# Kernel tuning notes

Measured on AMD Instinct MI355X. Metric: run time of the kernel, lower is better.

Reference implementation:

```python
import jax, jax.numpy as jnp
import numpy as np

HEADS = 8
KEY_DIM = 32
EPS = 1e-5


def layernorm(x, gamma, beta, eps=EPS):
    mu = jnp.mean(x, axis=-1, keepdims=True)
    var = jnp.mean(jnp.square(x - mu), axis=-1, keepdims=True)
    return (x - mu) * jax.lax.rsqrt(var + eps) * gamma + beta


def setup_inputs() -> dict:
    key = jax.random.key(0)
    ks = jax.random.split(key, 6)
    B, H, W, C = 16, 32, 32, 256
    inner = HEADS * KEY_DIM  # 256
    s = 1.0 / np.sqrt(C)
    return {
        "x": jax.random.normal(ks[0], (B, H, W, C), jnp.float32),
        "gamma": jnp.ones((C,), jnp.float32),
        "beta": jnp.zeros((C,), jnp.float32),
        "Wq": jax.random.normal(ks[1], (C, inner), jnp.float32) * s,
        "bq": jnp.zeros((inner,), jnp.float32),
        "Wk": jax.random.normal(ks[2], (C, inner), jnp.float32) * s,
        "bk": jnp.zeros((inner,), jnp.float32),
        "Wv": jax.random.normal(ks[3], (C, inner), jnp.float32) * s,
        "bv": jnp.zeros((inner,), jnp.float32),
        "Wp": jax.random.normal(ks[4], (inner, C), jnp.float32) * s,
        "bp": jnp.zeros((C,), jnp.float32),
    }


def reference(x, gamma, beta, Wq, bq, Wk, bk, Wv, bv, Wp, bp):
    B, H, W, C = x.shape
    N = H * W
    h, d = HEADS, KEY_DIM
    X = layernorm(x, gamma, beta)              # [B,H,W,C]
    Xf = X.reshape(B, N, C)                    # 1x1 conv == per-token linear
    Q = (Xf @ Wq + bq).reshape(B, N, h, d)
    K = (Xf @ Wk + bk).reshape(B, N, h, d)
    V = (Xf @ Wv + bv).reshape(B, N, h, d)
    scale = jnp.asarray(d, x.dtype) ** -0.5
    scores = jnp.einsum('bnhd,bmhd->bhnm', Q, K) * scale
    A = jax.nn.softmax(scores, axis=-1)        # [B,h,N,N]
    Y = jnp.einsum('bhnm,bmhd->bnhd', A, V).reshape(B, N, h * d)
    out = (Y @ Wp + bp).reshape(B, H, W, C)
    return out
```

## Files before the change

kernel.cpp:

```cpp
#include <hip/hip_runtime.h>
#include <hip/hip_bf16.h>

typedef __bf16 bf16_t;
typedef __attribute__((ext_vector_type(8))) __bf16 bf16x8;
typedef __attribute__((ext_vector_type(4))) float f32x4;
typedef __attribute__((ext_vector_type(4))) short s16x4;

#define GLDS16(g, l) __builtin_amdgcn_global_load_lds( \
    (const __attribute__((address_space(1))) unsigned int*)(g), \
    (__attribute__((address_space(3))) unsigned int*)(l), 16, 0, 0)

__device__ __forceinline__ float fexp2(float x) {
#if __has_builtin(__builtin_amdgcn_exp2f)
  return __builtin_amdgcn_exp2f(x);
#else
  return exp2f(x);
#endif
}

#define QSCALE (0.17677669529663688f * 1.4426950408889634f)

__global__ __launch_bounds__(256) void lnwtr_kernel(
    const float* __restrict__ x, const float* __restrict__ gamma,
    const float* __restrict__ beta, bf16_t* __restrict__ Xln,
    const float* __restrict__ Wq, const float* __restrict__ Wk,
    const float* __restrict__ Wv, const float* __restrict__ Wp,
    bf16_t* __restrict__ Wt)
{
  if (blockIdx.x < 1024) {
    const int idx = blockIdx.x * 256 + threadIdx.x;
    const int mat = idx >> 16;
    const int e   = idx & 65535;
    const int k   = e >> 8;
    const int n   = e & 255;
    const float* W = (mat == 0) ? Wq : (mat == 1) ? Wk : (mat == 2) ? Wv : Wp;
    Wt[(size_t)mat * 65536 + n * 256 + k] = (bf16_t)W[e];
    return;
  }
  const int wave = threadIdx.x >> 6, lane = threadIdx.x & 63;
  const int tok = (blockIdx.x - 1024) * 4 + wave;
  const float4 v = *reinterpret_cast<const float4*>(x + (size_t)tok * 256 + lane * 4);
  float s1 = v.x + v.y + v.z + v.w;
  float s2 = v.x*v.x + v.y*v.y + v.z*v.z + v.w*v.w;
  #pragma unroll
  for (int off = 1; off < 64; off <<= 1) {
    s1 += __shfl_xor(s1, off);
    s2 += __shfl_xor(s2, off);
  }
  const float mean = s1 * (1.0f/256.0f);
  const float var  = s2 * (1.0f/256.0f) - mean*mean;
  const float rstd = rsqrtf(var + 1e-5f);
  const float4 g  = *reinterpret_cast<const float4*>(gamma + lane*4);
  const float4 be = *reinterpret_cast<const float4*>(beta  + lane*4);
  union { bf16_t h4[4]; unsigned long long u; } pk;
  pk.h4[0] = (bf16_t)((v.x-mean)*rstd*g.x + be.x);
  pk.h4[1] = (bf16_t)((v.y-mean)*rstd*g.y + be.y);
  pk.h4[2] = (bf16_t)((v.z-mean)*rstd*g.z + be.z);
  pk.h4[3] = (bf16_t)((v.w-mean)*rstd*g.w + be.w);
  *reinterpret_cast<unsigned long long*>(Xln + (size_t)tok*256 + lane*4) = pk.u;
}

template<int MODE>
__global__ __launch_bounds__(256) void gemm_kernel(
    const bf16_t* __restrict__ A, const bf16_t* __restrict__ Wt,
    const float* __restrict__ b0, const float* __restrict__ b1,
    const float* __restrict__ b2,
    bf16_t* __restrict__ Qb, bf16_t* __restrict__ Kb, bf16_t* __restrict__ Vt,
    float* __restrict__ Fout)
{
  __shared__ __align__(16) bf16_t As[128*64];
  __shared__ __align__(16) bf16_t Bs[128*64];
  const int tid  = threadIdx.x;
  const int lane = tid & 63, wave = tid >> 6;
  const int lg = lane >> 4, li = lane & 15;
  const int wm = wave >> 1, wn = wave & 1;
  const int mt = blockIdx.x;
  const int nt = blockIdx.y;
  int mat, nbase;
  const bf16_t* Bm;
  if (MODE == 0) { mat = nt >> 1; nbase = (nt & 1) * 128; Bm = Wt + (size_t)mat * 65536; }
  else           { mat = 3;       nbase = nt * 128;       Bm = Wt; }

  f32x4 acc[4][4] = {};

  for (int kt = 0; kt < 4; ++kt) {
    __syncthreads();
    #pragma unroll
    for (int i = 0; i < 4; ++i) {
      const int idx = i*256 + tid;
      const int row = idx >> 3, ck = idx & 7;
      const int cs = ck ^ (row & 7);
      GLDS16(A + (size_t)(mt*128 + row)*256 + kt*64 + cs*8, As + idx*8);
    }
    #pragma unroll
    for (int i = 0; i < 4; ++i) {
      const int idx = i*256 + tid;
      const int row = idx >> 3, ck = idx & 7;
      const int cs = ck ^ (row & 7);
      GLDS16(Bm + (size_t)(nbase + row)*256 + kt*64 + cs*8, Bs + idx*8);
    }
    __syncthreads();
    #pragma unroll
    for (int kk = 0; kk < 2; ++kk) {
      bf16x8 af[4], bfv[4];
      #pragma unroll
      for (int mi = 0; mi < 4; ++mi) {
        const int row = wm*64 + mi*16 + li;
        const int c = (kk*4 + lg) ^ (row & 7);
        af[mi] = *reinterpret_cast<const bf16x8*>(As + row*64 + c*8);
      }
      #pragma unroll
      for (int ni = 0; ni < 4; ++ni) {
        const int row = wn*64 + ni*16 + li;
        const int c = (kk*4 + lg) ^ (row & 7);
        bfv[ni] = *reinterpret_cast<const bf16x8*>(Bs + row*64 + c*8);
      }
      #pragma unroll
      for (int mi = 0; mi < 4; ++mi)
        #pragma unroll
        for (int ni = 0; ni < 4; ++ni)
          acc[mi][ni] = __builtin_amdgcn_mfma_f32_16x16x32_bf16(af[mi], bfv[ni], acc[mi][ni], 0, 0, 0);
    }
  }

  if (MODE == 0) {
    const float* bias = (mat == 0) ? b0 : (mat == 1) ? b1 : b2;
    if (mat < 2) {
      bf16_t* Out = (mat == 0) ? Qb : Kb;
      const float osc = (mat == 0) ? QSCALE : 1.0f;
      #pragma unroll
      for (int mi = 0; mi < 4; ++mi)
        #pragma unroll
        for (int ni = 0; ni < 4; ++ni) {
          const int col = nbase + wn*64 + ni*16 + li;
          const float bb = bias[col];
          #pragma unroll
          for (int r = 0; r < 4; ++r) {
            const int row = mt*128 + wm*64 + mi*16 + lg*4 + r;
            Out[(size_t)row*256 + col] = (bf16_t)((acc[mi][ni][r] + bb) * osc);
          }
        }
    } else {
      #pragma unroll
      for (int mi = 0; mi < 4; ++mi)
        #pragma unroll
        for (int ni = 0; ni < 4; ++ni) {
          const int col = nbase + wn*64 + ni*16 + li;
          const int hh = col >> 5, dd = col & 31;
          const float bb = bias[col];
          const int row0 = mt*128 + wm*64 + mi*16 + lg*4;
          const int bi = row0 >> 10, nn = row0 & 1023;
          union { bf16_t h4[4]; unsigned long long u; } pk;
          #pragma unroll
          for (int r = 0; r < 4; ++r) pk.h4[r] = (bf16_t)(acc[mi][ni][r] + bb);
          *reinterpret_cast<unsigned long long*>(
              Vt + ((size_t)(bi*8 + hh)*32 + dd)*1024 + nn) = pk.u;
        }
    }
  } else {
    #pragma unroll
    for (int mi = 0; mi < 4; ++mi)
      #pragma unroll
      for (int ni = 0; ni < 4; ++ni) {
        const int col = nbase + wn*64 + ni*16 + li;
        const float bb = b0[col];
        #pragma unroll
        for (int r = 0; r < 4; ++r) {
          const int row = mt*128 + wm*64 + mi*16 + lg*4 + r;
          Fout[(size_t)row*256 + col] = acc[mi][ni][r] + bb;
        }
      }
  }
}

__global__ __launch_bounds__(512, 8) void attn_kernel(
    const bf16_t* __restrict__ Qb, const bf16_t* __restrict__ Kb,
    const bf16_t* __restrict__ Vt, bf16_t* __restrict__ Yb)
{
  __shared__ __align__(16) char Ks[3][4096];
  __shared__ __align__(16) char Vs[3][4096];
  const int tid  = threadIdx.x;
  const int wave = tid >> 6, lane = tid & 63;
  const int lg = lane >> 4, li = lane & 15;
  const int gid = blockIdx.x;
  const int qt = (gid >> 3) & 7;
  const int bh = ((gid >> 6) << 3) | (gid & 7);
  const int b  = bh >> 3, hh = bh & 7;
  const int tok0 = b*1024 + qt*128 + wave*16;

  const bf16x8 qf = *reinterpret_cast<const bf16x8*>(
      Qb + (size_t)(tok0 + li)*256 + hh*32 + lg*8);

  const bf16_t* Ssrc;
  if (tid < 256) {
    const int s = tid, ktok = s >> 2, ks = s & 3;
    Ssrc = Kb + (size_t)(b*1024 + ktok)*256 + hh*32 + ((ks ^ ((ktok >> 1) & 3)) * 8);
  } else {
    const int s = tid - 256, vd = s >> 3, vs = s & 7;
    Ssrc = Vt + ((size_t)bh*32 + vd)*1024 + ((vs ^ (vd & 7)) * 8);
  }
  const size_t sstride = (tid < 256) ? (size_t)16384 : (size_t)64;
  const int sloff = (tid < 256) ? tid*16 : (tid-256)*16;
  char* sbase = (tid < 256) ? &Ks[0][0] : &Vs[0][0];

  const int kof = li*64 + ((lg ^ ((li >> 1) & 3)) * 16);
  int vof[4];
  #pragma unroll
  for (int ct = 0; ct < 4; ++ct)
    vof[ct] = li*128 + (((ct*2 + (lg >> 1)) ^ (li & 7)) * 16) + (lg & 1)*8;

  const f32x4 fz = {0.f, 0.f, 0.f, 0.f};
  f32x4 acc0 = fz, acc1 = fz;
  f32x4 accl = fz;
  float m = 0.f;
  bool bump = false;

  const short oneb = 0x3F80;
  const s16x4 vone = {oneb, oneb, oneb, oneb};

  GLDS16(Ssrc,           sbase + sloff);
  GLDS16(Ssrc + sstride, sbase + 4096 + sloff);

  #pragma unroll
  for (int mc = 0; mc < 16; ++mc) {
    if (mc < 15) asm volatile("s_waitcnt vmcnt(1)" ::: "memory");
    else         asm volatile("s_waitcnt vmcnt(0)" ::: "memory");
    __builtin_amdgcn_s_barrier();
    asm volatile("" ::: "memory");
    if (mc + 2 < 16)
      GLDS16(Ssrc + (size_t)(mc+2)*sstride, sbase + ((mc+2)%3)*4096 + sloff);
    const char* kb = &Ks[mc%3][0];
    const char* vb = &Vs[mc%3][0];
    f32x4 s[4];
    #pragma unroll
    for (int ct = 0; ct < 4; ++ct) {
      const bf16x8 kfrag = *reinterpret_cast<const bf16x8*>(kb + kof + ct*1024);
      s[ct] = __builtin_amdgcn_mfma_f32_16x16x32_bf16(kfrag, qf, fz, 0, 0, 0);
    }
    const float mxa = fmaxf(fmaxf(s[0][0], s[0][1]), fmaxf(s[0][2], s[0][3]));
    const float mxb = fmaxf(fmaxf(s[1][0], s[1][1]), fmaxf(s[1][2], s[1][3]));
    const float mxc = fmaxf(fmaxf(s[2][0], s[2][1]), fmaxf(s[2][2], s[2][3]));
    const float mxd = fmaxf(fmaxf(s[3][0], s[3][1]), fmaxf(s[3][2], s[3][3]));
    const float pmax = fmaxf(fmaxf(mxa, mxb), fmaxf(mxc, mxd));
    if (!__all(pmax - m <= 8.0f)) {
      float rmx = fmaxf(pmax, __shfl_xor(pmax, 16));
      rmx = fmaxf(rmx, __shfl_xor(rmx, 32));
      const float mnew = fmaxf(m, rmx);
      const float sf = fexp2(m - mnew);
      #pragma unroll
      for (int r = 0; r < 4; ++r) { acc0[r] *= sf; acc1[r] *= sf; accl[r] *= sf; }
      m = mnew; bump = true;
    }
    #pragma unroll
    for (int ct = 0; ct < 4; ++ct) {
      union { bf16_t h4[4]; s16x4 v; } pk;
      if (!bump) {
        #pragma unroll
        for (int r = 0; r < 4; ++r) pk.h4[r] = (bf16_t)fexp2(s[ct][r]);
      } else {
        #pragma unroll
        for (int r = 0; r < 4; ++r) pk.h4[r] = (bf16_t)fexp2(s[ct][r] - m);
      }
      const s16x4 vq0 = *reinterpret_cast<const s16x4*>(vb + vof[ct]);
      const s16x4 vq1 = *reinterpret_cast<const s16x4*>(vb + vof[ct] + 16*128);
      acc0 = __builtin_amdgcn_mfma_f32_16x16x16bf16_1k(vq0,  pk.v, acc0, 0, 0, 0);
      acc1 = __builtin_amdgcn_mfma_f32_16x16x16bf16_1k(vq1,  pk.v, acc1, 0, 0, 0);
      accl = __builtin_amdgcn_mfma_f32_16x16x16bf16_1k(vone, pk.v, accl, 0, 0, 0);
    }
  }

  const float inv = 1.0f / accl[0];
  union { bf16_t h4[4]; unsigned long long u; } o0, o1;
  #pragma unroll
  for (int r = 0; r < 4; ++r) {
    o0.h4[r] = (bf16_t)(acc0[r]*inv);
    o1.h4[r] = (bf16_t)(acc1[r]*inv);
  }
  bf16_t* yp = Yb + (size_t)(tok0 + li)*256 + hh*32;
  *reinterpret_cast<unsigned long long*>(yp + lg*4)      = o0.u;
  *reinterpret_cast<unsigned long long*>(yp + 16 + lg*4) = o1.u;
}

extern "C" void kernel_launch(void* const* d_in, const int* in_sizes, int n_in,
                              void* d_out, int out_size, void* d_ws, size_t ws_size,
                              hipStream_t stream) {
  const float* x     = (const float*)d_in[0];
  const float* gamma = (const float*)d_in[1];
  const float* beta  = (const float*)d_in[2];
  const float* Wq    = (const float*)d_in[3];
  const float* bq    = (const float*)d_in[4];
  const float* Wk    = (const float*)d_in[5];
  const float* bk    = (const float*)d_in[6];
  const float* Wv    = (const float*)d_in[7];
  const float* bv    = (const float*)d_in[8];
  const float* Wp    = (const float*)d_in[9];
  const float* bp    = (const float*)d_in[10];
  float* out = (float*)d_out;

  char* ws = (char*)d_ws;
  bf16_t* Wt  = (bf16_t*)(ws);
  bf16_t* Xln = (bf16_t*)(ws + 524288);
  bf16_t* Qb  = (bf16_t*)(ws + 8912896);
  bf16_t* Kb  = (bf16_t*)(ws + 17301504);
  bf16_t* Vt  = (bf16_t*)(ws + 25690112);
  bf16_t* Yb  = Xln;

  lnwtr_kernel<<<5120, 256, 0, stream>>>(x, gamma, beta, Xln,
                                         Wq, Wk, Wv, Wp, Wt);
  gemm_kernel<0><<<dim3(128, 6), 256, 0, stream>>>(
      Xln, Wt, bq, bk, bv, Qb, Kb, Vt, nullptr);
  attn_kernel<<<1024, 512, 0, stream>>>(Qb, Kb, Vt, Yb);
  gemm_kernel<1><<<dim3(128, 2), 256, 0, stream>>>(
      Yb, Wt + 3*65536, bp, nullptr, nullptr, nullptr, nullptr, nullptr, out);
}
```

Baseline: 72.03 us.

## Rewrite attention kernel with 32x32 MFMA tiles and 4 waves per block

Restructures the attention kernel to use 32x32x16 bf16 MFMA, so each wave now handles 32 query rows instead of 16, and blocks shrink from 8 to 4 waves. The row sum is kept in registers with a VALU reduction, replacing the extra ones-vector MFMA. P is repacked through cross-half lane shuffles to form the B operand. All threads now issue both K and V global-to-LDS loads. The aim is higher MFMA efficiency and fewer redundant matrix ops. The cost is extra shuffles, more register pressure, and fewer waves per block.

```diff
diff --git a/kernel.cpp b/kernel.cpp
--- a/kernel.cpp
+++ b/kernel.cpp
@@ -4,7 +4,7 @@
 typedef __bf16 bf16_t;
 typedef __attribute__((ext_vector_type(8))) __bf16 bf16x8;
 typedef __attribute__((ext_vector_type(4))) float f32x4;
-typedef __attribute__((ext_vector_type(4))) short s16x4;
+typedef __attribute__((ext_vector_type(16))) float f32x16;
 
 #define GLDS16(g, l) __builtin_amdgcn_global_load_lds( \
     (const __attribute__((address_space(1))) unsigned int*)(g), \
@@ -173,7 +173,7 @@
   }
 }
 
-__global__ __launch_bounds__(512, 8) void attn_kernel(
+__global__ __launch_bounds__(256, 4) void attn_kernel(
     const bf16_t* __restrict__ Qb, const bf16_t* __restrict__ Kb,
     const bf16_t* __restrict__ Vt, bf16_t* __restrict__ Yb)
 {
@@ -181,104 +181,147 @@
   __shared__ __align__(16) char Vs[3][4096];
   const int tid  = threadIdx.x;
   const int wave = tid >> 6, lane = tid & 63;
-  const int lg = lane >> 4, li = lane & 15;
+  const int q = lane & 31, half = lane >> 5;
   const int gid = blockIdx.x;
   const int qt = (gid >> 3) & 7;
   const int bh = ((gid >> 6) << 3) | (gid & 7);
   const int b  = bh >> 3, hh = bh & 7;
-  const int tok0 = b*1024 + qt*128 + wave*16;
-
-  const bf16x8 qf = *reinterpret_cast<const bf16x8*>(
-      Qb + (size_t)(tok0 + li)*256 + hh*32 + lg*8);
-
-  const bf16_t* Ssrc;
-  if (tid < 256) {
-    const int s = tid, ktok = s >> 2, ks = s & 3;
-    Ssrc = Kb + (size_t)(b*1024 + ktok)*256 + hh*32 + ((ks ^ ((ktok >> 1) & 3)) * 8);
-  } else {
-    const int s = tid - 256, vd = s >> 3, vs = s & 7;
-    Ssrc = Vt + ((size_t)bh*32 + vd)*1024 + ((vs ^ (vd & 7)) * 8);
-  }
-  const size_t sstride = (tid < 256) ? (size_t)16384 : (size_t)64;
-  const int sloff = (tid < 256) ? tid*16 : (tid-256)*16;
-  char* sbase = (tid < 256) ? &Ks[0][0] : &Vs[0][0];
-
-  const int kof = li*64 + ((lg ^ ((li >> 1) & 3)) * 16);
-  int vof[4];
-  #pragma unroll
-  for (int ct = 0; ct < 4; ++ct)
-    vof[ct] = li*128 + (((ct*2 + (lg >> 1)) ^ (li & 7)) * 16) + (lg & 1)*8;
-
-  const f32x4 fz = {0.f, 0.f, 0.f, 0.f};
-  f32x4 acc0 = fz, acc1 = fz;
-  f32x4 accl = fz;
+  const int tok0 = b*1024 + qt*128 + wave*32;
+
+  const bf16_t* qrow = Qb + (size_t)(tok0 + q)*256 + hh*32 + half*8;
+  const bf16x8 qf0 = *reinterpret_cast<const bf16x8*>(qrow);
+  const bf16x8 qf1 = *reinterpret_cast<const bf16x8*>(qrow + 16);
+
+  const int kt_ = tid >> 2, ks_ = tid & 3;
+  const bf16_t* Ksrc = Kb + (size_t)(b*1024 + kt_)*256 + hh*32
+                          + ((ks_ ^ ((kt_ >> 1) & 3)) * 8);
+  const int vd_ = tid >> 3, vs_ = tid & 7;
+  const bf16_t* Vsrc = Vt + ((size_t)bh*32 + vd_)*1024 + ((vs_ ^ (vd_ & 7)) * 8);
+
+  int koff[2][2];
+  #pragma unroll
+  for (int g = 0; g < 2; ++g)
+    #pragma unroll
+    for (int h = 0; h < 2; ++h)
+      koff[g][h] = (g*32 + q)*64 + (((h*2 + half) ^ ((q >> 1) & 3)) << 4);
+  int voff[4];
+  #pragma unroll
+  for (int i = 0; i < 4; ++i)
+    voff[i] = q*128 + (((i*2 + half) ^ (q & 7)) << 4);
+
+  const f32x16 z16 = {0,0,0,0,0,0,0,0,0,0,0,0,0,0,0,0};
+  f32x16 acc = z16;
   float m = 0.f;
+  float lrow = 0.f;
   bool bump = false;
 
-  const short oneb = 0x3F80;
-  const s16x4 vone = {oneb, oneb, oneb, oneb};
-
-  GLDS16(Ssrc,           sbase + sloff);
-  GLDS16(Ssrc + sstride, sbase + 4096 + sloff);
+  GLDS16(Ksrc,         &Ks[0][tid*16]);
+  GLDS16(Vsrc,         &Vs[0][tid*16]);
+  GLDS16(Ksrc + 16384, &Ks[1][tid*16]);
+  GLDS16(Vsrc + 64,    &Vs[1][tid*16]);
 
   #pragma unroll
   for (int mc = 0; mc < 16; ++mc) {
-    if (mc < 15) asm volatile("s_waitcnt vmcnt(1)" ::: "memory");
+    if (mc < 15) asm volatile("s_waitcnt vmcnt(2)" ::: "memory");
     else         asm volatile("s_waitcnt vmcnt(0)" ::: "memory");
     __builtin_amdgcn_s_barrier();
     asm volatile("" ::: "memory");
-    if (mc + 2 < 16)
-      GLDS16(Ssrc + (size_t)(mc+2)*sstride, sbase + ((mc+2)%3)*4096 + sloff);
+    if (mc + 2 < 16) {
+      GLDS16(Ksrc + (size_t)(mc+2)*16384, &Ks[(mc+2)%3][tid*16]);
+      GLDS16(Vsrc + (mc+2)*64,            &Vs[(mc+2)%3][tid*16]);
+    }
     const char* kb = &Ks[mc%3][0];
     const char* vb = &Vs[mc%3][0];
-    f32x4 s[4];
-    #pragma unroll
-    for (int ct = 0; ct < 4; ++ct) {
-      const bf16x8 kfrag = *reinterpret_cast<const bf16x8*>(kb + kof + ct*1024);
-      s[ct] = __builtin_amdgcn_mfma_f32_16x16x32_bf16(kfrag, qf, fz, 0, 0, 0);
-    }
-    const float mxa = fmaxf(fmaxf(s[0][0], s[0][1]), fmaxf(s[0][2], s[0][3]));
-    const float mxb = fmaxf(fmaxf(s[1][0], s[1][1]), fmaxf(s[1][2], s[1][3]));
-    const float mxc = fmaxf(fmaxf(s[2][0], s[2][1]), fmaxf(s[2][2], s[2][3]));
-    const float mxd = fmaxf(fmaxf(s[3][0], s[3][1]), fmaxf(s[3][2], s[3][3]));
-    const float pmax = fmaxf(fmaxf(mxa, mxb), fmaxf(mxc, mxd));
-    if (!__all(pmax - m <= 8.0f)) {
-      float rmx = fmaxf(pmax, __shfl_xor(pmax, 16));
-      rmx = fmaxf(rmx, __shfl_xor(rmx, 32));
-      const float mnew = fmaxf(m, rmx);
-      const float sf = fexp2(m - mnew);
-      #pragma unroll
-      for (int r = 0; r < 4; ++r) { acc0[r] *= sf; acc1[r] *= sf; accl[r] *= sf; }
-      m = mnew; bump = true;
-    }
-    #pragma unroll
-    for (int ct = 0; ct < 4; ++ct) {
-      union { bf16_t h4[4]; s16x4 v; } pk;
-      if (!bump) {
-        #pragma unroll
-        for (int r = 0; r < 4; ++r) pk.h4[r] = (bf16_t)fexp2(s[ct][r]);
-      } else {
-        #pragma unroll
-        for (int r = 0; r < 4; ++r) pk.h4[r] = (bf16_t)fexp2(s[ct][r] - m);
-      }
-      const s16x4 vq0 = *reinterpret_cast<const s16x4*>(vb + vof[ct]);
-      const s16x4 vq1 = *reinterpret_cast<const s16x4*>(vb + vof[ct] + 16*128);
-      acc0 = __builtin_amdgcn_mfma_f32_16x16x16bf16_1k(vq0,  pk.v, acc0, 0, 0, 0);
-      acc1 = __builtin_amdgcn_mfma_f32_16x16x16bf16_1k(vq1,  pk.v, acc1, 0, 0, 0);
-      accl = __builtin_amdgcn_mfma_f32_16x16x16bf16_1k(vone, pk.v, accl, 0, 0, 0);
-    }
-  }
-
-  const float inv = 1.0f / accl[0];
-  union { bf16_t h4[4]; unsigned long long u; } o0, o1;
-  #pragma unroll
-  for (int r = 0; r < 4; ++r) {
-    o0.h4[r] = (bf16_t)(acc0[r]*inv);
-    o1.h4[r] = (bf16_t)(acc1[r]*inv);
-  }
-  bf16_t* yp = Yb + (size_t)(tok0 + li)*256 + hh*32;
-  *reinterpret_cast<unsigned long long*>(yp + lg*4)      = o0.u;
-  *reinterpret_cast<unsigned long long*>(yp + 16 + lg*4) = o1.u;
+    f32x16 s0, s1;
+    {
+      const bf16x8 k00 = *reinterpret_cast<const bf16x8*>(kb + koff[0][0]);
+      const bf16x8 k01 = *reinterpret_cast<const bf16x8*>(kb + koff[0][1]);
+      s0 = __builtin_amdgcn_mfma_f32_32x32x16_bf16(k00, qf0, z16, 0, 0, 0);
+      s0 = __builtin_amdgcn_mfma_f32_32x32x16_bf16(k01, qf1, s0, 0, 0, 0);
+      const bf16x8 k10 = *reinterpret_cast<const bf16x8*>(kb + koff[1][0]);
+      const bf16x8 k11 = *reinterpret_cast<const bf16x8*>(kb + koff[1][1]);
+      s1 = __builtin_amdgcn_mfma_f32_32x32x16_bf16(k10, qf0, z16, 0, 0, 0);
+      s1 = __builtin_amdgcn_mfma_f32_32x32x16_bf16(k11, qf1, s1, 0, 0, 0);
+    }
+    {
+      float mx[16];
+      #pragma unroll
+      for (int j = 0; j < 16; ++j) mx[j] = fmaxf(s0[j], s1[j]);
+      #pragma unroll
+      for (int st = 8; st > 0; st >>= 1)
+        #pragma unroll
+        for (int j = 0; j < st; ++j) mx[j] = fmaxf(mx[j], mx[j+st]);
+      const float pmax = mx[0];
+      if (!__all(pmax - m <= 8.0f)) {
+        float rmx = fmaxf(pmax, __shfl_xor(pmax, 16));
+        rmx = fmaxf(rmx, __shfl_xor(rmx, 32));
+        rmx = fmaxf(rmx, __shfl_xor(rmx, 8));
+        rmx = fmaxf(rmx, __shfl_xor(rmx, 4));
+        rmx = fmaxf(rmx, __shfl_xor(rmx, 2));
+        rmx = fmaxf(rmx, __shfl_xor(rmx, 1));
+        const float mnew = fmaxf(m, rmx);
+        const float sf = fexp2(m - mnew);
+        #pragma unroll
+        for (int r = 0; r < 16; ++r) acc[r] *= sf;
+        lrow *= sf;
+        m = mnew; bump = true;
+      }
+    }
+    if (!bump) {
+      #pragma unroll
+      for (int j = 0; j < 16; ++j) { s0[j] = fexp2(s0[j]); s1[j] = fexp2(s1[j]); }
+    } else {
+      #pragma unroll
+      for (int j = 0; j < 16; ++j) { s0[j] = fexp2(s0[j] - m); s1[j] = fexp2(s1[j] - m); }
+    }
+    {
+      float ad[16];
+      #pragma unroll
+      for (int j = 0; j < 16; ++j) ad[j] = s0[j] + s1[j];
+      #pragma unroll
+      for (int st = 8; st > 0; st >>= 1)
+        #pragma unroll
+        for (int j = 0; j < st; ++j) ad[j] += ad[j+st];
+      lrow += ad[0];
+    }
+    unsigned w0[4][2], w1[4][2];
+    #pragma unroll
+    for (int t = 0; t < 4; ++t)
+      #pragma unroll
+      for (int u = 0; u < 2; ++u) {
+        union { bf16_t h[2]; unsigned w; } pa, pb;
+        pa.h[0] = (bf16_t)s0[4*t + 2*u]; pa.h[1] = (bf16_t)s0[4*t + 2*u + 1];
+        pb.h[0] = (bf16_t)s1[4*t + 2*u]; pb.h[1] = (bf16_t)s1[4*t + 2*u + 1];
+        w0[t][u] = pa.w; w1[t][u] = pb.w;
+      }
+    #pragma unroll
+    for (int i = 0; i < 4; ++i) {
+      const int tp = (i & 1) * 2;
+      union { unsigned w[4]; bf16x8 v; } pf;
+      #pragma unroll
+      for (int u = 0; u < 2; ++u) {
+        const unsigned Au = (i >> 1) ? w1[tp][u]     : w0[tp][u];
+        const unsigned Bu = (i >> 1) ? w1[tp + 1][u] : w0[tp + 1][u];
+        const unsigned Cu = half ? Au : Bu;
+        const unsigned Ru = (unsigned)__shfl_xor((int)Cu, 32);
+        pf.w[u]     = half ? Ru : Au;
+        pf.w[2 + u] = half ? Bu : Ru;
+      }
+      const bf16x8 vfrag = *reinterpret_cast<const bf16x8*>(vb + voff[i]);
+      acc = __builtin_amdgcn_mfma_f32_32x32x16_bf16(vfrag, pf.v, acc, 0, 0, 0);
+    }
+  }
+
+  const float lsum = lrow + __shfl_xor(lrow, 32);
+  const float inv = 1.0f / lsum;
+  bf16_t* yp = Yb + (size_t)(tok0 + q)*256 + hh*32 + 4*half;
+  #pragma unroll
+  for (int t = 0; t < 4; ++t) {
+    union { bf16_t h4[4]; unsigned long long u; } o;
+    #pragma unroll
+    for (int j = 0; j < 4; ++j) o.h4[j] = (bf16_t)(acc[4*t + j] * inv);
+    *reinterpret_cast<unsigned long long*>(yp + 8*t) = o.u;
+  }
 }
 
 extern "C" void kernel_launch(void* const* d_in, const int* in_sizes, int n_in,
@@ -309,7 +352,7 @@
                                          Wq, Wk, Wv, Wp, Wt);
   gemm_kernel<0><<<dim3(128, 6), 256, 0, stream>>>(
       Xln, Wt, bq, bk, bv, Qb, Kb, Vt, nullptr);
-  attn_kernel<<<1024, 512, 0, stream>>>(Qb, Kb, Vt, Yb);
+  attn_kernel<<<1024, 256, 0, stream>>>(Qb, Kb, Vt, Yb);
   gemm_kernel<1><<<dim3(128, 2), 256, 0, stream>>>(
       Yb, Wt + 3*65536, bp, nullptr, nullptr, nullptr, nullptr, nullptr, out);
 }
```

Result: slower. 77.70 us (+7.9%).
